# Kernel optimization log

Hardware: AMD Instinct MI355X
Metric: run time of the kernel (lower is better)

## Reference

```python
import jax, jax.numpy as jnp
import numpy as np

NEG_SLOPE = 0.2


def setup_inputs() -> dict:
    key = jax.random.key(0)
    ks = jax.random.split(key, 7)
    N, E, F_IN, H, D = 100000, 1600000, 256, 4, 64
    feat = jax.random.normal(ks[0], (N, F_IN), dtype=jnp.float32)
    W = jax.random.normal(ks[1], (F_IN, H * D), dtype=jnp.float32) * (1.0 / np.sqrt(F_IN))
    attn_l = jax.random.normal(ks[2], (H, D), dtype=jnp.float32) * 0.1
    attn_r = jax.random.normal(ks[3], (H, D), dtype=jnp.float32) * 0.1
    bias = jnp.zeros((H * D,), dtype=jnp.float32)
    src = jax.random.randint(ks[4], (E,), 0, N, dtype=jnp.int32)
    dst = jax.random.randint(ks[5], (E,), 0, N, dtype=jnp.int32)
    return {"feat": feat, "W": W, "attn_l": attn_l, "attn_r": attn_r,
            "bias": bias, "src": src, "dst": dst}


def reference(feat, W, attn_l, attn_r, bias, src, dst):
    N = feat.shape[0]
    H, D = attn_l.shape
    # fc: [N, F_in] @ [F_in, H*D] -> [N, H, D]
    h = (feat @ W).reshape(N, H, D)
    # per-node attention logits (dot with attn vectors): [N, H]
    el = jnp.einsum('nhd,hd->nh', h, attn_l)
    er = jnp.einsum('nhd,hd->nh', h, attn_r)
    # edge scores: e_ij = LeakyReLU(el[src] + er[dst]) -> [E, H]
    e = el[src] + er[dst]
    e = jnp.where(e > 0, e, NEG_SLOPE * e)
    # segment softmax over destination neighborhoods
    e_max = jax.ops.segment_max(e, dst, num_segments=N)          # [N, H]
    e_max = jnp.where(jnp.isfinite(e_max), e_max, 0.0)           # guard 0-in-degree
    e_exp = jnp.exp(e - e_max[dst])                              # [E, H]
    denom = jax.ops.segment_sum(e_exp, dst, num_segments=N)      # [N, H]
    a = e_exp / jnp.maximum(denom[dst], 1e-16)                   # [E, H]
    # weighted scatter-add of source messages: [E, H, D] -> [N, H, D]
    msg = h[src] * a[:, :, None]
    out = jax.ops.segment_sum(msg, dst, num_segments=N)
    out = out + bias.reshape(1, H, D)
    return out
```

## Files before the change

### kernel.cpp

```cpp
#include <hip/hip_runtime.h>
#include <hip/hip_bf16.h>
#include <math.h>

#define HEADS 4
#define DHEAD 64
#define HD 256
#define F_IN 256
#define NEG_SLOPE 0.2f

typedef __attribute__((ext_vector_type(8))) short bf16x8;
typedef __attribute__((ext_vector_type(8))) ushort u16x8;
typedef __attribute__((ext_vector_type(4))) float f32x4;

__device__ __forceinline__ ushort f2bf(float f) {
    __hip_bfloat16 b = __float2bfloat16(f);
    ushort u; __builtin_memcpy(&u, &b, 2);
    return u;
}

#define HIST_BLOCKS 3072
__global__ __launch_bounds__(256) void prep_k(const float* __restrict__ W,
                                              ushort* __restrict__ Wt,
                                              const int* __restrict__ dst,
                                              int* __restrict__ counts,
                                              ushort* __restrict__ pos, int E) {
    if (blockIdx.x < 256) {
        int i = blockIdx.x * 256 + threadIdx.x;
        int k = i >> 8, c = i & 255;
        int ct = c >> 4, kb = k >> 5, kh = (k >> 3) & 3, j = k & 7;
        int l = kh * 16 + (c & 15);
        Wt[(size_t)((ct * 8 + kb) * 64 + l) * 8 + j] = f2bf(W[i]);
    } else {
        const int stride = HIST_BLOCKS * 256;
        for (int i = (blockIdx.x - 256) * 256 + threadIdx.x; i < E; i += stride)
            pos[i] = (ushort)atomicAdd(&counts[dst[i]], 1);
    }
}

__global__ __launch_bounds__(256) void gemm_k(const float* __restrict__ A,
                                              const ushort* __restrict__ Wt,
                                              const float* __restrict__ attn_l,
                                              const float* __restrict__ attn_r,
                                              ushort* __restrict__ hbf,
                                              float* __restrict__ el,
                                              float* __restrict__ er, int M) {
    __shared__ ushort As[64 * 256];
    const int tid = threadIdx.x;
    const int wave = tid >> 6;
    const int lane = tid & 63;
    const int r16 = lane & 15;
    const int khalf = lane >> 4;
    const int row0 = blockIdx.x * 64;
    const int wcol0 = wave * 64;

    bf16x8 b[4][8];
#pragma unroll
    for (int nc = 0; nc < 4; ++nc) {
        const int ct = wave * 4 + nc;
#pragma unroll
        for (int kb = 0; kb < 8; ++kb)
            b[nc][kb] = *(const bf16x8*)(Wt + ((size_t)(ct * 8 + kb) * 64 + lane) * 8);
    }

    {
        const int srow = tid >> 2;
        const int cg = tid & 3;
        int arow = row0 + srow; if (arow >= M) arow = M - 1;
        const float* ap = A + (size_t)arow * F_IN + cg * 64;
        const int sw = (srow & 7) << 4;
        char* wb = (char*)As + srow * 512;
#pragma unroll
        for (int q = 0; q < 8; ++q) {
            float4 f0 = *(const float4*)(ap + q * 8);
            float4 f1 = *(const float4*)(ap + q * 8 + 4);
            u16x8 cv;
            cv[0] = f2bf(f0.x); cv[1] = f2bf(f0.y); cv[2] = f2bf(f0.z); cv[3] = f2bf(f0.w);
            cv[4] = f2bf(f1.x); cv[5] = f2bf(f1.y); cv[6] = f2bf(f1.z); cv[7] = f2bf(f1.w);
            *(u16x8*)(wb + ((cg * 128 + q * 16) ^ sw)) = cv;
        }
    }
    __syncthreads();

    f32x4 acc[4][4] = {};
#pragma unroll
    for (int kb = 0; kb < 8; ++kb) {
        bf16x8 a[4];
#pragma unroll
        for (int mr = 0; mr < 4; ++mr) {
            const int row = mr * 16 + r16;
            const int sw = (row & 7) << 4;
            a[mr] = *(const bf16x8*)((const char*)As + row * 512 +
                                     ((kb * 64 + khalf * 16) ^ sw));
        }
#pragma unroll
        for (int mr = 0; mr < 4; ++mr)
#pragma unroll
            for (int nc = 0; nc < 4; ++nc)
                acc[mr][nc] = __builtin_amdgcn_mfma_f32_16x16x32_bf16(
                    a[mr], b[nc][kb], acc[mr][nc], 0, 0, 0);
    }

    float al[4], ar[4];
#pragma unroll
    for (int nc = 0; nc < 4; ++nc) {
        al[nc] = attn_l[wcol0 + nc * 16 + r16];
        ar[nc] = attn_r[wcol0 + nc * 16 + r16];
    }
#pragma unroll
    for (int mr = 0; mr < 4; ++mr) {
#pragma unroll
        for (int r = 0; r < 4; ++r) {
            int row = row0 + mr * 16 + khalf * 4 + r;
            float vl = 0.f, vr = 0.f;
#pragma unroll
            for (int nc = 0; nc < 4; ++nc) {
                float v = acc[mr][nc][r];
                vl = fmaf(v, al[nc], vl);
                vr = fmaf(v, ar[nc], vr);
            }
#pragma unroll
            for (int off = 1; off < 16; off <<= 1) {
                vl += __shfl_xor(vl, off);
                vr += __shfl_xor(vr, off);
            }
            if (row < M) {
                if (r16 == 0) {
                    el[row * HEADS + wave] = vl;
                    er[row * HEADS + wave] = vr;
                }
#pragma unroll
                for (int nc = 0; nc < 4; ++nc)
                    hbf[(size_t)row * HD + wcol0 + nc * 16 + r16] = f2bf(acc[mr][nc][r]);
            }
        }
    }
}

#define SCAN_SPAN 4096
__global__ __launch_bounds__(1024) void blocksum_k(const int* __restrict__ counts,
                                                   int* __restrict__ btot, int N) {
    __shared__ int wsum[16];
    const int tid = threadIdx.x, lane = tid & 63, wid = tid >> 6;
    int i0 = blockIdx.x * SCAN_SPAN + tid * 4;
    int t = 0;
#pragma unroll
    for (int r = 0; r < 4; ++r) { int i = i0 + r; if (i < N) t += counts[i]; }
#pragma unroll
    for (int off = 32; off; off >>= 1) t += __shfl_xor(t, off);
    if (lane == 0) wsum[wid] = t;
    __syncthreads();
    if (tid == 0) {
        int s = 0;
        for (int w = 0; w < 16; ++w) s += wsum[w];
        btot[blockIdx.x] = s;
    }
}

__global__ __launch_bounds__(64) void scanb_k(const int* __restrict__ btot,
                                              int* __restrict__ boff, int nb) {
    int lane = threadIdx.x;
    int v = (lane < nb) ? btot[lane] : 0;
    int sc = v;
    for (int off = 1; off < 64; off <<= 1) {
        int u = __shfl_up(sc, off);
        if (lane >= off) sc += u;
    }
    if (lane < nb) boff[lane] = sc - v;
}

__global__ __launch_bounds__(1024) void scanw_k(const int* __restrict__ counts,
                                                const int* __restrict__ boff,
                                                int* __restrict__ row_start, int N) {
    __shared__ int wsum[16];
    const int tid = threadIdx.x, lane = tid & 63, wid = tid >> 6;
    int i0 = blockIdx.x * SCAN_SPAN + tid * 4;
    int v[4]; int t = 0;
#pragma unroll
    for (int r = 0; r < 4; ++r) { int i = i0 + r; v[r] = (i < N) ? counts[i] : 0; t += v[r]; }
    int sc = t;
    for (int off = 1; off < 64; off <<= 1) {
        int u = __shfl_up(sc, off);
        if (lane >= off) sc += u;
    }
    if (lane == 63) wsum[wid] = sc;
    __syncthreads();
    int wpref = 0;
    for (int w = 0; w < wid; ++w) wpref += wsum[w];
    int excl = boff[blockIdx.x] + wpref + sc - t;
    int run = 0;
#pragma unroll
    for (int r = 0; r < 4; ++r) {
        int i = i0 + r;
        if (i < N) row_start[i] = excl + run;
        run += v[r];
    }
    if (N - 1 >= i0 && N - 1 < i0 + 4) row_start[N] = excl + run;
}

__global__ __launch_bounds__(256) void place_k(const int* __restrict__ src,
                                               const int* __restrict__ dst,
                                               const ushort* __restrict__ pos,
                                               const int* __restrict__ row_start,
                                               int* __restrict__ sorted_src, int E) {
    int i = blockIdx.x * 256 + threadIdx.x;
    if (i < E)
        sorted_src[row_start[dst[i]] + (int)pos[i]] = src[i];
}

__global__ __launch_bounds__(256) void gat4_k(const ushort* __restrict__ hbf,
                                              const float* __restrict__ el,
                                              const float* __restrict__ er,
                                              const float* __restrict__ bias,
                                              const int* __restrict__ row_start,
                                              const int* __restrict__ sorted_src,
                                              float* __restrict__ out, int N) {
    __shared__ int   s_idx[4][64];
    __shared__ float p_s[4][64][4];
    const int wv = threadIdx.x >> 6, lane = threadIdx.x & 63;
    const int head = lane >> 4;
    const int n = blockIdx.x * 4 + wv;
    if (n >= N) return;

    const int start = row_start[n], end = row_start[n + 1];
    const int deg = end - start;

    const float4 er4 = *(const float4*)&er[n * 4];
    const ushort* __restrict__ hrow = hbf + (unsigned)lane * 4u;

    float acc0 = 0.f, acc1 = 0.f, acc2 = 0.f, acc3 = 0.f, ssum = 0.f;

#define GLOAD(i, V, Q) { int s_ = s_idx[wv][i]; Q = p_s[wv][i][head]; \
                         V = *(const uint2*)(hrow + (size_t)(unsigned)s_ * HD); }
#define GUSE(V, Q) { union { unsigned u; float f; } b0_, b1_, b2_, b3_; \
                     b0_.u = V.x << 16; b1_.u = V.x & 0xffff0000u; \
                     b2_.u = V.y << 16; b3_.u = V.y & 0xffff0000u; \
                     acc0 = fmaf(Q, b0_.f, acc0); acc1 = fmaf(Q, b1_.f, acc1); \
                     acc2 = fmaf(Q, b2_.f, acc2); acc3 = fmaf(Q, b3_.f, acc3); \
                     ssum += Q; }

    for (int c0 = 0; c0 < deg; c0 += 64) {
        const int cnt = min(64, deg - c0);
        if (lane < cnt) {
            int s = sorted_src[start + c0 + lane];
            float4 e4 = *(const float4*)&el[s * 4];
            float4 pv;
            float x0 = e4.x + er4.x; x0 = fmaxf(x0, NEG_SLOPE * x0);
            float x1 = e4.y + er4.y; x1 = fmaxf(x1, NEG_SLOPE * x1);
            float x2 = e4.z + er4.z; x2 = fmaxf(x2, NEG_SLOPE * x2);
            float x3 = e4.w + er4.w; x3 = fmaxf(x3, NEG_SLOPE * x3);
            pv.x = __expf(x0); pv.y = __expf(x1); pv.z = __expf(x2); pv.w = __expf(x3);
            s_idx[wv][lane] = s;
            *(float4*)&p_s[wv][lane][0] = pv;
        }
        __builtin_amdgcn_wave_barrier();

        int k = 0;
        if (cnt >= 16) {
            uint2 V[8]; float Q[8];
#pragma unroll
            for (int j = 0; j < 8; ++j) GLOAD(j, V[j], Q[j]);
            for (; k + 16 <= cnt; k += 8) {
#pragma unroll
                for (int j = 0; j < 8; ++j) { GUSE(V[j], Q[j]); GLOAD(k + 8 + j, V[j], Q[j]); }
            }
#pragma unroll
            for (int j = 0; j < 8; ++j) GUSE(V[j], Q[j]);
            k += 8;
        } else if (cnt >= 8) {
            uint2 va, vb, vc, vd; float qa, qb, qc, qd;
            GLOAD(0, va, qa); GLOAD(1, vb, qb); GLOAD(2, vc, qc); GLOAD(3, vd, qd);
            for (; k + 8 <= cnt; k += 4) {
                GUSE(va, qa); GLOAD(k + 4, va, qa);
                GUSE(vb, qb); GLOAD(k + 5, vb, qb);
                GUSE(vc, qc); GLOAD(k + 6, vc, qc);
                GUSE(vd, qd); GLOAD(k + 7, vd, qd);
            }
            GUSE(va, qa); GUSE(vb, qb); GUSE(vc, qc); GUSE(vd, qd);
            k += 4;
        }
        for (; k < cnt; ++k) { uint2 v; float q; GLOAD(k, v, q); GUSE(v, q); }
        __builtin_amdgcn_wave_barrier();
    }
#undef GLOAD
#undef GUSE

    const float inv = 1.0f / fmaxf(ssum, 1e-16f);
    const float4 b4 = *(const float4*)&bias[lane * 4];
    float4 o;
    o.x = fmaf(acc0, inv, b4.x);
    o.y = fmaf(acc1, inv, b4.y);
    o.z = fmaf(acc2, inv, b4.z);
    o.w = fmaf(acc3, inv, b4.w);
    *(float4*)&out[(size_t)n * HD + lane * 4] = o;
}

extern "C" void kernel_launch(void* const* d_in, const int* in_sizes, int n_in,
                              void* d_out, int out_size, void* d_ws, size_t ws_size,
                              hipStream_t stream) {
    const float* feat   = (const float*)d_in[0];
    const float* W      = (const float*)d_in[1];
    const float* attn_l = (const float*)d_in[2];
    const float* attn_r = (const float*)d_in[3];
    const float* bias   = (const float*)d_in[4];
    const int*   src    = (const int*)d_in[5];
    const int*   dst    = (const int*)d_in[6];

    const int N = in_sizes[0] / F_IN;
    const int E = in_sizes[5];

    ushort* hbf = (ushort*)d_ws;
    float* el = (float*)(hbf + (size_t)N * HD);
    float* er = el + (size_t)N * HEADS;
    int* counts     = (int*)(er + (size_t)N * HEADS);
    int* row_start  = counts + N;
    int* sorted_src = row_start + (N + 1);
    int* btot       = sorted_src + E;
    int* boff       = btot + 64;
    ushort* pos     = (ushort*)(boff + 64);
    ushort* Wt = (ushort*)(((uintptr_t)(pos + E) + 15) & ~(uintptr_t)15);

    float* out = (float*)d_out;

    const int nb = (N + SCAN_SPAN - 1) / SCAN_SPAN;

    hipMemsetAsync(counts, 0, (size_t)N * sizeof(int), stream);
    prep_k<<<256 + HIST_BLOCKS, 256, 0, stream>>>(W, Wt, dst, counts, pos, E);
    gemm_k<<<(N + 63) / 64, 256, 0, stream>>>(feat, Wt, attn_l, attn_r, hbf, el, er, N);

    blocksum_k<<<nb, 1024, 0, stream>>>(counts, btot, N);
    scanb_k<<<1, 64, 0, stream>>>(btot, boff, nb);
    scanw_k<<<nb, 1024, 0, stream>>>(counts, boff, row_start, N);
    place_k<<<(E + 255) / 256, 256, 0, stream>>>(src, dst, pos, row_start, sorted_src, E);

    gat4_k<<<(N + 3) / 4, 256, 0, stream>>>(hbf, el, er, bias, row_start, sorted_src, out, N);
}
```

Measured before the change: 320.3 us.

## Fuse three-pass scan into one kernel and run one wave per node in aggregation

The separate blocksum, block-offset scan and local scan kernels become a single scan kernel. Each block now recomputes its own prefix by summing every count before its span, which removes two launches but adds redundant reads of counts. The aggregation kernel now launches one 64-thread block per destination node instead of four waves per 256-thread block. Its 8-deep software-pipelined gather path is dropped, so only the 4-deep path remains, which lowers register use but exposes less memory-level parallelism for high-degree nodes.

```diff
diff --git a/kernel.cpp b/kernel.cpp
--- a/kernel.cpp
+++ b/kernel.cpp
@@ -137,43 +137,28 @@
 }
 
 #define SCAN_SPAN 4096
-__global__ __launch_bounds__(1024) void blocksum_k(const int* __restrict__ counts,
-                                                   int* __restrict__ btot, int N) {
+__global__ __launch_bounds__(1024) void scan1_k(const int* __restrict__ counts,
+                                                int* __restrict__ row_start, int N) {
     __shared__ int wsum[16];
+    __shared__ int s_pref;
     const int tid = threadIdx.x, lane = tid & 63, wid = tid >> 6;
-    int i0 = blockIdx.x * SCAN_SPAN + tid * 4;
-    int t = 0;
-#pragma unroll
-    for (int r = 0; r < 4; ++r) { int i = i0 + r; if (i < N) t += counts[i]; }
-#pragma unroll
-    for (int off = 32; off; off >>= 1) t += __shfl_xor(t, off);
-    if (lane == 0) wsum[wid] = t;
+    const int base = blockIdx.x * SCAN_SPAN;
+
+    int pref = 0;
+    for (int i = tid; i < base; i += 1024) pref += counts[i];
+#pragma unroll
+    for (int off = 32; off; off >>= 1) pref += __shfl_xor(pref, off);
+    if (lane == 0) wsum[wid] = pref;
     __syncthreads();
     if (tid == 0) {
         int s = 0;
+#pragma unroll
         for (int w = 0; w < 16; ++w) s += wsum[w];
-        btot[blockIdx.x] = s;
-    }
-}
-
-__global__ __launch_bounds__(64) void scanb_k(const int* __restrict__ btot,
-                                              int* __restrict__ boff, int nb) {
-    int lane = threadIdx.x;
-    int v = (lane < nb) ? btot[lane] : 0;
-    int sc = v;
-    for (int off = 1; off < 64; off <<= 1) {
-        int u = __shfl_up(sc, off);
-        if (lane >= off) sc += u;
-    }
-    if (lane < nb) boff[lane] = sc - v;
-}
-
-__global__ __launch_bounds__(1024) void scanw_k(const int* __restrict__ counts,
-                                                const int* __restrict__ boff,
-                                                int* __restrict__ row_start, int N) {
-    __shared__ int wsum[16];
-    const int tid = threadIdx.x, lane = tid & 63, wid = tid >> 6;
-    int i0 = blockIdx.x * SCAN_SPAN + tid * 4;
+        s_pref = s;
+    }
+    __syncthreads();
+
+    int i0 = base + tid * 4;
     int v[4]; int t = 0;
 #pragma unroll
     for (int r = 0; r < 4; ++r) { int i = i0 + r; v[r] = (i < N) ? counts[i] : 0; t += v[r]; }
@@ -182,11 +167,12 @@
         int u = __shfl_up(sc, off);
         if (lane >= off) sc += u;
     }
+    __syncthreads();
     if (lane == 63) wsum[wid] = sc;
     __syncthreads();
     int wpref = 0;
     for (int w = 0; w < wid; ++w) wpref += wsum[w];
-    int excl = boff[blockIdx.x] + wpref + sc - t;
+    int excl = s_pref + wpref + sc - t;
     int run = 0;
 #pragma unroll
     for (int r = 0; r < 4; ++r) {
@@ -207,19 +193,18 @@
         sorted_src[row_start[dst[i]] + (int)pos[i]] = src[i];
 }
 
-__global__ __launch_bounds__(256) void gat4_k(const ushort* __restrict__ hbf,
-                                              const float* __restrict__ el,
-                                              const float* __restrict__ er,
-                                              const float* __restrict__ bias,
-                                              const int* __restrict__ row_start,
-                                              const int* __restrict__ sorted_src,
-                                              float* __restrict__ out, int N) {
-    __shared__ int   s_idx[4][64];
-    __shared__ float p_s[4][64][4];
-    const int wv = threadIdx.x >> 6, lane = threadIdx.x & 63;
+__global__ __launch_bounds__(64) void gat4_k(const ushort* __restrict__ hbf,
+                                             const float* __restrict__ el,
+                                             const float* __restrict__ er,
+                                             const float* __restrict__ bias,
+                                             const int* __restrict__ row_start,
+                                             const int* __restrict__ sorted_src,
+                                             float* __restrict__ out, int N) {
+    __shared__ int   s_idx[64];
+    __shared__ float p_s[64][4];
+    const int lane = threadIdx.x;
     const int head = lane >> 4;
-    const int n = blockIdx.x * 4 + wv;
-    if (n >= N) return;
+    const int n = blockIdx.x;
 
     const int start = row_start[n], end = row_start[n + 1];
     const int deg = end - start;
@@ -229,7 +214,7 @@
 
     float acc0 = 0.f, acc1 = 0.f, acc2 = 0.f, acc3 = 0.f, ssum = 0.f;
 
-#define GLOAD(i, V, Q) { int s_ = s_idx[wv][i]; Q = p_s[wv][i][head]; \
+#define GLOAD(i, V, Q) { int s_ = s_idx[i]; Q = p_s[i][head]; \
                          V = *(const uint2*)(hrow + (size_t)(unsigned)s_ * HD); }
 #define GUSE(V, Q) { union { unsigned u; float f; } b0_, b1_, b2_, b3_; \
                      b0_.u = V.x << 16; b1_.u = V.x & 0xffff0000u; \
@@ -249,24 +234,13 @@
             float x2 = e4.z + er4.z; x2 = fmaxf(x2, NEG_SLOPE * x2);
             float x3 = e4.w + er4.w; x3 = fmaxf(x3, NEG_SLOPE * x3);
             pv.x = __expf(x0); pv.y = __expf(x1); pv.z = __expf(x2); pv.w = __expf(x3);
-            s_idx[wv][lane] = s;
-            *(float4*)&p_s[wv][lane][0] = pv;
+            s_idx[lane] = s;
+            *(float4*)&p_s[lane][0] = pv;
         }
         __builtin_amdgcn_wave_barrier();
 
         int k = 0;
-        if (cnt >= 16) {
-            uint2 V[8]; float Q[8];
-#pragma unroll
-            for (int j = 0; j < 8; ++j) GLOAD(j, V[j], Q[j]);
-            for (; k + 16 <= cnt; k += 8) {
-#pragma unroll
-                for (int j = 0; j < 8; ++j) { GUSE(V[j], Q[j]); GLOAD(k + 8 + j, V[j], Q[j]); }
-            }
-#pragma unroll
-            for (int j = 0; j < 8; ++j) GUSE(V[j], Q[j]);
-            k += 8;
-        } else if (cnt >= 8) {
+        if (cnt >= 8) {
             uint2 va, vb, vc, vd; float qa, qb, qc, qd;
             GLOAD(0, va, qa); GLOAD(1, vb, qb); GLOAD(2, vc, qc); GLOAD(3, vd, qd);
             for (; k + 8 <= cnt; k += 4) {
@@ -314,9 +288,7 @@
     int* counts     = (int*)(er + (size_t)N * HEADS);
     int* row_start  = counts + N;
     int* sorted_src = row_start + (N + 1);
-    int* btot       = sorted_src + E;
-    int* boff       = btot + 64;
-    ushort* pos     = (ushort*)(boff + 64);
+    ushort* pos     = (ushort*)(sorted_src + E);
     ushort* Wt = (ushort*)(((uintptr_t)(pos + E) + 15) & ~(uintptr_t)15);
 
     float* out = (float*)d_out;
@@ -327,10 +299,8 @@
     prep_k<<<256 + HIST_BLOCKS, 256, 0, stream>>>(W, Wt, dst, counts, pos, E);
     gemm_k<<<(N + 63) / 64, 256, 0, stream>>>(feat, Wt, attn_l, attn_r, hbf, el, er, N);
 
-    blocksum_k<<<nb, 1024, 0, stream>>>(counts, btot, N);
-    scanb_k<<<1, 64, 0, stream>>>(btot, boff, nb);
-    scanw_k<<<nb, 1024, 0, stream>>>(counts, boff, row_start, N);
+    scan1_k<<<nb, 1024, 0, stream>>>(counts, row_start, N);
     place_k<<<(E + 255) / 256, 256, 0, stream>>>(src, dst, pos, row_start, sorted_src, E);
 
-    gat4_k<<<(N + 3) / 4, 256, 0, stream>>>(hbf, el, er, bias, row_start, sorted_src, out, N);
-}
+    gat4_k<<<N, 64, 0, stream>>>(hbf, el, er, bias, row_start, sorted_src, out, N);
+}
```

Measured after the change: 327.6 us. 2.3% more time.
